# Kernel tuning notes

Hardware: AMD Instinct MI355X
Metric: run time of the kernel (lower is better)

Reference implementation:

```python
import jax, jax.numpy as jnp
import numpy as np

N, D = 4096, 512
TAU, ALPHA, EPS = 0.2, 0.5, 1e-15
L2_EPS = 1e-12  # F.normalize eps


def setup_inputs() -> dict:
    key = jax.random.key(0)
    ks = jax.random.split(key, 12)
    # xavier_normal_ with gain=1.414 for [D, D] linears
    std = 1.414 * (2.0 / (D + D)) ** 0.5
    xn = lambda k: jax.random.normal(k, (D, D), jnp.float32) * std
    return {
        "z1": jax.random.normal(ks[0], (N, D), jnp.float32),
        "z2": jax.random.normal(ks[1], (N, D), jnp.float32),
        # local projector: Linear -> PReLU -> Linear
        "lw1": xn(ks[2]), "lb1": jnp.zeros((D,), jnp.float32),
        "la": jnp.full((1,), 0.25, jnp.float32),  # PReLU weight (torch default 0.25)
        "lw2": xn(ks[3]), "lb2": jnp.zeros((D,), jnp.float32),
        # global projector
        "gw1": xn(ks[4]), "gb1": jnp.zeros((D,), jnp.float32),
        "ga": jnp.full((1,), 0.25, jnp.float32),
        "gw2": xn(ks[5]), "gb2": jnp.zeros((D,), jnp.float32),
        # discriminator bilinear weight
        "W": xn(ks[6]),
        # binary positive-pair mask [N, N]
        "mask": jax.random.randint(ks[7], (N, N), 0, 2, jnp.int32),
    }


def _prelu(x, a):
    return jnp.where(x >= 0, x, a * x)


def _proj(z, w1, b1, a, w2, b2):
    # nn.Sequential(Linear, PReLU, Linear); torch Linear: z @ W.T + b
    return _prelu(z @ w1.T + b1, a[0]) @ w2.T + b2


def _l2norm(z):
    n = jnp.linalg.norm(z, axis=-1, keepdims=True)
    return z / jnp.maximum(n, L2_EPS)


def _infonce(h1, h2, m, tau):
    a = _l2norm(h1)
    b = _l2norm(h2)
    sim_intra = jnp.exp(a @ a.T / tau)  # [N, N]
    sim_inter = jnp.exp(a @ b.T / tau)  # [N, N]
    num = (sim_inter * m).sum(1)
    den = sim_intra.sum(1) + sim_inter.sum(1) - (sim_intra * m).sum(1)
    return (-jnp.log(num / den)).mean()


def reference(z1, z2, lw1, lb1, la, lw2, lb2, gw1, gb1, ga, gw2, gb2, W, mask):
    m = mask.astype(jnp.float32)
    # local (node-level) InfoNCE through the local projector
    h1 = _proj(z1, lw1, lb1, la, lw2, lb2)
    h2 = _proj(z2, lw1, lb1, la, lw2, lb2)
    local = 0.5 * (_infonce(h1, h2, m, TAU) + _infonce(h2, h1, m.T, TAU))

    # global (DGI-style) loss
    def gloss(pos_z, neg_z):
        s = pos_z.mean(0)                               # readout [D]
        h = _proj(s, gw1, gb1, ga, gw2, gb2)            # global projector [D]
        summ = W @ h                                    # [D]
        d_pos = jax.nn.sigmoid(pos_z @ summ)            # [N]
        d_neg = jax.nn.sigmoid(neg_z @ summ)            # [N]
        pos_loss = -jnp.log(d_pos + EPS).mean()
        neg_loss = -jnp.log(1.0 - d_neg + EPS).mean()
        return 0.5 * (pos_loss + neg_loss)

    glob = 0.5 * (gloss(z1, z2) + gloss(z2, z1))
    return ALPHA * local + (1.0 - ALPHA) * glob
```

## Files before the change

kernel.cpp:

```cpp
#include <hip/hip_runtime.h>
#include <math.h>

#define NN 4096
#define DD 512
#define INV_TAU 5.0f
#define EPSV 1e-15f

typedef unsigned short u16;
typedef unsigned long long u64;
typedef __attribute__((ext_vector_type(8))) short short8;
typedef __attribute__((ext_vector_type(4))) float f32x4;

__device__ __forceinline__ void gld16(const void* g, void* l) {
  __builtin_amdgcn_global_load_lds(
      (const __attribute__((address_space(1))) unsigned int*)g,
      (__attribute__((address_space(3))) unsigned int*)l, 16, 0, 0);
}

__device__ __forceinline__ void bar_vm4() {
  asm volatile("s_waitcnt vmcnt(4) lgkmcnt(0)\n\ts_barrier" ::: "memory");
}
__device__ __forceinline__ void bar_vm2() {
  asm volatile("s_waitcnt vmcnt(2) lgkmcnt(0)\n\ts_barrier" ::: "memory");
}
__device__ __forceinline__ void bar_vm1() {
  asm volatile("s_waitcnt vmcnt(1) lgkmcnt(0)\n\ts_barrier" ::: "memory");
}
__device__ __forceinline__ void bar_vm0() {
  asm volatile("s_waitcnt vmcnt(0) lgkmcnt(0)\n\ts_barrier" ::: "memory");
}

__device__ __forceinline__ float bf2f(u16 u) {
  return __uint_as_float(((unsigned)u) << 16);
}
__device__ __forceinline__ u16 f2bf(float x) {
  unsigned u = __float_as_uint(x);
  u += 0x7fff + ((u >> 16) & 1);
  return (u16)(u >> 16);
}

__device__ __forceinline__ float wave_sum(float v) {
#pragma unroll
  for (int o = 32; o > 0; o >>= 1) v += __shfl_down(v, o, 64);
  return v;
}

__device__ __forceinline__ float ldz(const float* p) {
  return __hip_atomic_load(p, __ATOMIC_RELAXED, __HIP_MEMORY_SCOPE_AGENT);
}
__device__ __forceinline__ void stz(float* p, float v) {
  __hip_atomic_store(p, v, __ATOMIC_RELAXED, __HIP_MEMORY_SCOPE_AGENT);
}

__device__ __forceinline__ void fin_run(const float* zb, const float* plsP,
                                        const float* plsN, float* out,
                                        int tid) {
  const int lane = tid & 63, w = tid >> 6;
  float S1 = 0.f, S2 = 0.f;
#pragma unroll
  for (int k = 0; k < 8; ++k) {
    const int i = tid + k * 512;
    const float r11 = ldz(&zb[i]), r11m = ldz(&zb[NN + i]);
    const float r12 = ldz(&zb[2 * NN + i]), r12m = ldz(&zb[3 * NN + i]);
    const float c12 = ldz(&zb[4 * NN + i]), c12m = ldz(&zb[5 * NN + i]);
    const float c22 = ldz(&zb[6 * NN + i]), c22m = ldz(&zb[7 * NN + i]);
    S1 += -logf(r12m / (r11 + r12 - r11m));
    S2 += -logf(c12m / (c22 + c12 - c22m));
  }
  float G = (tid < 64) ? (ldz(&plsP[tid]) + ldz(&plsN[tid])) : 0.f;
  S1 = wave_sum(S1);
  S2 = wave_sum(S2);
  G = wave_sum(G);
  __shared__ float fr[3][8];
  if (lane == 0) { fr[0][w] = S1; fr[1][w] = S2; fr[2][w] = G; }
  __syncthreads();
  if (tid == 0) {
    float s1t = 0.f, s2t = 0.f, gt = 0.f;
    for (int q = 0; q < 8; ++q) {
      s1t += fr[0][q];
      s2t += fr[1][q];
      gt += fr[2][q];
    }
    const float local = 0.5f * (s1t + s2t) * (1.f / NN);
    const float glob = 0.25f * gt * (1.f / NN);
    out[0] = 0.5f * local + 0.5f * glob;
  }
}

__global__ __launch_bounds__(256) void tobf16cm(
    const float* __restrict__ a, const float* __restrict__ b,
    const float* __restrict__ c, const float* __restrict__ d2,
    u16* __restrict__ o, float* __restrict__ pc1, float* __restrict__ pc2,
    float* __restrict__ zbf, int* __restrict__ ctr) {
  const int bid = blockIdx.x, tid = threadIdx.x;
  if (bid >= 4608) {
    const int blk = bid - 4608;
    const int r0 = blk * 32;
    float a0 = 0.f, a1 = 0.f, c0 = 0.f, c1 = 0.f;
    for (int r = r0; r < r0 + 32; ++r) {
      const size_t ro = (size_t)r * DD;
      a0 += c[ro + tid];
      a1 += c[ro + 256 + tid];
      c0 += d2[ro + tid];
      c1 += d2[ro + 256 + tid];
    }
    pc1[blk * 512 + tid] = a0;
    pc1[blk * 512 + 256 + tid] = a1;
    pc2[blk * 512 + tid] = c0;
    pc2[blk * 512 + 256 + tid] = c1;
    return;
  }
  if (bid == 0 && tid == 0) ctr[0] = 0;
  if (bid < 128) zbf[bid * 256 + tid] = 0.f;
  const int i = bid * 256 + tid;
  int j = i;
  const float* s;
  if (j < 65536) {
    s = a + (size_t)j * 4;
  } else {
    j -= 65536;
    if (j < 65536) {
      s = b + (size_t)j * 4;
    } else {
      j -= 65536;
      if (j < 524288) {
        s = c + (size_t)j * 4;
      } else {
        j -= 524288;
        s = d2 + (size_t)j * 4;
      }
    }
  }
  float4 v = *(const float4*)s;
  u64 pk = (u64)f2bf(v.x) | ((u64)f2bf(v.y) << 16) | ((u64)f2bf(v.z) << 32) |
           ((u64)f2bf(v.w) << 48);
  *(u64*)&o[(size_t)i * 4] = pk;
}

template <int ACT>
__global__ __launch_bounds__(512) void gemm_mv(
    const u16* __restrict__ A, const u16* __restrict__ Bw,
    const float* __restrict__ bias, const float* __restrict__ alpha_p,
    u16* __restrict__ out, const float* __restrict__ Mw,
    const float* __restrict__ mx1, const float* __restrict__ mx2,
    const float* __restrict__ mbias, const float* __restrict__ mal,
    float* __restrict__ my1, float* __restrict__ my2) {
  __shared__ __align__(16) u16 sh[3 * 6144];
  __shared__ float svb[512];
  const int tid = threadIdx.x, w = tid >> 6, lane = tid & 63;
  if (blockIdx.x < 64) {
    const int mb = blockIdx.x;
    const int bz = mb >> 5, bx = mb & 31;
    const float* xin = bz ? mx2 : mx1;
    float* y = bz ? my2 : my1;
    if (ACT) {
      float a0 = 0.f, a1 = 0.f, a2 = 0.f, a3 = 0.f;
      for (int b = 0; b < 128; b += 4) {
        a0 += xin[b * 512 + tid];
        a1 += xin[(b + 1) * 512 + tid];
        a2 += xin[(b + 2) * 512 + tid];
        a3 += xin[(b + 3) * 512 + tid];
      }
      svb[tid] = ((a0 + a1) + (a2 + a3)) * (1.f / NN);
    } else {
      svb[tid] = xin[tid];
    }
    __syncthreads();
#pragma unroll
    for (int rr = 0; rr < 2; ++rr) {
      const int row = bx * 16 + w * 2 + rr;
      float acc = 0.f;
#pragma unroll
      for (int q = 0; q < 8; ++q)
        acc = fmaf(Mw[(size_t)row * DD + lane + 64 * q], svb[lane + 64 * q],
                   acc);
      acc = wave_sum(acc);
      if (lane == 0) {
        acc += mbias[row];
        if (ACT) {
          const float al = mal[0];
          acc = (acc >= 0.f) ? acc : al * acc;
        }
        y[row] = acc;
      }
    }
    return;
  }
  const int quad = lane >> 4, m16 = lane & 15;
  const int wi = w >> 1, wj = w & 1;
  const int bid2 = blockIdx.x - 64;
  const int xcd = bid2 & 7, idx = bid2 >> 3;
  const int i0 = (4 * xcd + (idx & 3)) * 128;
  const int j0 = ((idx >> 2) & 7) * 64;
  const int bz = idx >> 5;
  const u16* Ab = A + (size_t)bz * ((size_t)NN * DD);
  u16* ob = out + (size_t)bz * ((size_t)NN * DD);
  const int roff =
      (m16 >> 1) * 64 + (((((m16 & 1) << 2) | quad) ^ (m16 >> 1)) * 8);
  const int st = (lane & 7) ^ (lane >> 3);
  const int srow = 2 * (lane >> 3) + (st >> 2);
  const int scol = (st & 3) * 8;
  const u16* gs = (w < 4) ? Ab : Bw;
  const int grow0 = ((w < 4) ? i0 + 2 * w * 16 : j0 + (w - 4) * 16) + srow;
  const int doff0 = (w < 4) ? 2 * w * 512 : 4096 + (w - 4) * 512;
  auto stage = [&](int bo, int k) {
    const int kn = k * 32;
    gld16(&gs[(size_t)grow0 * DD + kn + scol], sh + bo + doff0);
    if (w < 4)
      gld16(&gs[(size_t)(grow0 + 16) * DD + kn + scol], sh + bo + doff0 + 512);
  };
  stage(0, 0);
  stage(6144, 1);
  if (w < 4) bar_vm2(); else bar_vm1();
  f32x4 acc[2][2] = {};
  int ro = 0;
  for (int kc = 0; kc < 16; ++kc) {
    if (kc <= 13) {
      int so = ro + 12288;
      if (so >= 18432) so -= 18432;
      stage(so, kc + 2);
    }
    const u16* As = sh + ro;
    const u16* Bs = sh + ro + 4096;
    short8 ar[2], br[2];
#pragma unroll
    for (int s = 0; s < 2; ++s) {
      ar[s] = *(const short8*)&As[(wi * 32 + s * 16) * 32 + roff];
      br[s] = *(const short8*)&Bs[(wj * 32 + s * 16) * 32 + roff];
    }
    __builtin_amdgcn_s_setprio(1);
#pragma unroll
    for (int si = 0; si < 2; ++si)
#pragma unroll
      for (int sj = 0; sj < 2; ++sj)
        acc[si][sj] = __builtin_amdgcn_mfma_f32_16x16x32_bf16(
            ar[si], br[sj], acc[si][sj], 0, 0, 0);
    __builtin_amdgcn_s_setprio(0);
    if (kc <= 13) {
      if (w < 4) bar_vm2(); else bar_vm1();
    } else if (kc == 14) {
      bar_vm0();
    }
    ro += 6144;
    if (ro == 18432) ro = 0;
  }
  const float al = ACT ? alpha_p[0] : 0.f;
#pragma unroll
  for (int si = 0; si < 2; ++si)
#pragma unroll
    for (int sj = 0; sj < 2; ++sj) {
      const int col = j0 + wj * 32 + sj * 16 + m16;
      const float bv = bias[col];
#pragma unroll
      for (int r = 0; r < 4; ++r) {
        const int row = i0 + wi * 32 + si * 16 + quad * 4 + r;
        float x = acc[si][sj][r] + bv;
        if (ACT) x = (x >= 0.f) ? x : al * x;
        ob[(size_t)row * DD + col] = f2bf(x);
      }
    }
}

__global__ __launch_bounds__(256) void rownorm_mv(
    const u16* __restrict__ h, u16* __restrict__ o,
    const float* __restrict__ W, const float* __restrict__ hx1,
    const float* __restrict__ hx2, float* __restrict__ sm1,
    float* __restrict__ sm2) {
  const int bid = blockIdx.x, tid = threadIdx.x;
  const int lane = tid & 63, w = tid >> 6;
  if (bid < 256) {
    const int bz = bid >> 7, bx = bid & 127;
    const float* x = bz ? hx2 : hx1;
    float* y = bz ? sm2 : sm1;
    const int row = bx * 4 + w;
    float acc = 0.f;
#pragma unroll
    for (int q = 0; q < 8; ++q)
      acc = fmaf(W[(size_t)row * DD + lane + 64 * q], x[lane + 64 * q], acc);
    acc = wave_sum(acc);
    if (lane == 0) y[row] = acc;
    return;
  }
  const int row = (bid - 256) * 4 + w;
  const size_t base = (size_t)row * DD + lane * 8;
  short8 v = *(const short8*)&h[base];
  float f[8];
  float s = 0.f;
#pragma unroll
  for (int j = 0; j < 8; ++j) {
    f[j] = bf2f((u16)v[j]);
    s += f[j] * f[j];
  }
  s = wave_sum(s);
  const float inv = 1.f / fmaxf(sqrtf(__shfl(s, 0, 64)), 1e-12f);
  short8 r;
#pragma unroll
  for (int j = 0; j < 8; ++j) r[j] = (short)f2bf(f[j] * inv);
  *(short8*)&o[base] = r;
}

__global__ __launch_bounds__(512) void sim_mfma(
    const u16* __restrict__ na, const u16* __restrict__ nb,
    const int* __restrict__ mask, float* __restrict__ zb,
    const float* __restrict__ z1g, const float* __restrict__ z2g,
    const float* __restrict__ sm1, const float* __restrict__ sm2,
    float* __restrict__ plsP, float* __restrict__ plsN,
    int* __restrict__ ctr, float* __restrict__ out) {
  extern __shared__ __align__(16) u16 shm[];
  __shared__ int lastf;
  const int tid = threadIdx.x;
  const int w = tid >> 6, lane = tid & 63;
  if (blockIdx.y < 2) {
    const int lx = blockIdx.y * 32 + blockIdx.x;
    const int bz = lx >> 5, bx5 = lx & 31;
    const float* z = bz ? z2g : z1g;
    const float* sp = bz ? sm2 : sm1;
    const float* sn = bz ? sm1 : sm2;
    float lp = 0.f, ln_ = 0.f;
    for (int k = 0; k < 16; ++k) {
      const int row = bx5 * 128 + w * 16 + k;
      float dp = 0.f, dn = 0.f;
#pragma unroll
      for (int t = 0; t < 8; ++t) {
        const float zv = z[(size_t)row * DD + lane + 64 * t];
        dp = fmaf(zv, sp[lane + 64 * t], dp);
        dn = fmaf(zv, sn[lane + 64 * t], dn);
      }
      dp = wave_sum(dp);
      dn = wave_sum(dn);
      if (lane == 0) {
        lp += -logf(1.f / (1.f + __expf(-dp)) + EPSV);
        ln_ += -logf(1.f - 1.f / (1.f + __expf(-dn)) + EPSV);
      }
    }
    float* red = (float*)shm;
    if (lane == 0) { red[w] = lp; red[8 + w] = ln_; }
    __syncthreads();
    if (tid == 0) {
      float sP = 0.f, sN = 0.f;
      for (int q = 0; q < 8; ++q) { sP += red[q]; sN += red[8 + q]; }
      stz(&plsP[lx], sP);
      stz(&plsN[lx], sN);
    }
    asm volatile("s_waitcnt vmcnt(0)" ::: "memory");
    __syncthreads();
    if (tid == 0) lastf = (atomicAdd(ctr, 1) == 1087) ? 1 : 0;
    __syncthreads();
    if (lastf) fin_run(zb, plsP, plsN, out, tid);
    return;
  }
  const int quad = lane >> 4, m16 = lane & 15;
  const int ig = w & 3, jh = w >> 2;
  const int i0 = (blockIdx.y - 2) * 128, j0 = blockIdx.x * 128;
  const int roff =
      (m16 >> 1) * 64 + (((((m16 & 1) << 2) | quad) ^ (m16 >> 1)) * 8);
  const int st = (lane & 7) ^ (lane >> 3);
  const int srow = 2 * (lane >> 3) + (st >> 2);
  const int scol = (st & 3) * 8;
  const int p = w >> 1, rh = (w & 1) * 64;
  const u16* gs = (p & 1) ? nb : na;
  const int gr = ((p < 2) ? i0 : j0) + rh + srow;
  u16* dst0 = shm + p * 4096 + rh * 32;
  auto stage = [&](int bo, int k) {
    const int kn = k * 32;
#pragma unroll
    for (int rr = 0; rr < 64; rr += 16)
      gld16(&gs[(size_t)(gr + rr) * DD + kn + scol], dst0 + bo + rr * 32);
  };
  stage(0, 0);
  stage(16384, 1);
  bar_vm4();
  f32x4 a11[2][4] = {}, a12[2][4] = {}, a22[2][4] = {};
  int ro = 0;
  for (int kc = 0; kc < 16; ++kc) {
    if (kc <= 13) {
      int so = ro + 32768;
      if (so >= 49152) so -= 49152;
      stage(so, kc + 2);
    }
    const u16* Ai = shm + ro;
    const u16* Bi = shm + ro + 4096;
    const u16* Aj = shm + ro + 8192;
    const u16* Bj = shm + ro + 12288;
    short8 ai0 = *(const short8*)&Ai[(ig * 32) * 32 + roff];
    short8 ai1 = *(const short8*)&Ai[(ig * 32 + 16) * 32 + roff];
    short8 bi0 = *(const short8*)&Bi[(ig * 32) * 32 + roff];
    short8 bi1 = *(const short8*)&Bi[(ig * 32 + 16) * 32 + roff];
#pragma unroll
    for (int c = 0; c < 4; ++c) {
      short8 aj = *(const short8*)&Aj[(jh * 64 + c * 16) * 32 + roff];
      short8 bj = *(const short8*)&Bj[(jh * 64 + c * 16) * 32 + roff];
      __builtin_amdgcn_s_setprio(1);
      a11[0][c] = __builtin_amdgcn_mfma_f32_16x16x32_bf16(ai0, aj, a11[0][c], 0, 0, 0);
      a11[1][c] = __builtin_amdgcn_mfma_f32_16x16x32_bf16(ai1, aj, a11[1][c], 0, 0, 0);
      a12[0][c] = __builtin_amdgcn_mfma_f32_16x16x32_bf16(ai0, bj, a12[0][c], 0, 0, 0);
      a12[1][c] = __builtin_amdgcn_mfma_f32_16x16x32_bf16(ai1, bj, a12[1][c], 0, 0, 0);
      a22[0][c] = __builtin_amdgcn_mfma_f32_16x16x32_bf16(bi0, bj, a22[0][c], 0, 0, 0);
      a22[1][c] = __builtin_amdgcn_mfma_f32_16x16x32_bf16(bi1, bj, a22[1][c], 0, 0, 0);
      __builtin_amdgcn_s_setprio(0);
    }
    if (kc <= 13) bar_vm4();
    else if (kc == 14) bar_vm0();
    ro += 16384;
    if (ro == 49152) ro = 0;
  }
  float* rred = (float*)(shm + 16384);
  float* cred = rred + 512;
  rred[tid] = 0.f;
  rred[tid + 512] = 0.f;
  __syncthreads();
  float rs11[2][4] = {}, rm11[2][4] = {}, rs12[2][4] = {}, rm12[2][4] = {};
  float cs12[4] = {}, cm12[4] = {}, cs22[4] = {}, cm22[4] = {};
#pragma unroll
  for (int t = 0; t < 2; ++t)
#pragma unroll
    for (int c = 0; c < 4; ++c) {
      const int gj = j0 + jh * 64 + c * 16 + m16;
#pragma unroll
      for (int r = 0; r < 4; ++r) {
        const int gi = i0 + ig * 32 + t * 16 + quad * 4 + r;
        const float mv = (float)mask[(size_t)gi * NN + gj];
        const float e11 = __expf(a11[t][c][r] * INV_TAU);
        const float e12 = __expf(a12[t][c][r] * INV_TAU);
        const float e22 = __expf(a22[t][c][r] * INV_TAU);
        rs11[t][r] += e11;
        rm11[t][r] += e11 * mv;
        rs12[t][r] += e12;
        rm12[t][r] += e12 * mv;
        cs12[c] += e12;
        cm12[c] += e12 * mv;
        cs22[c] += e22;
        cm22[c] += e22 * mv;
      }
    }
#pragma unroll
  for (int t = 0; t < 2; ++t)
#pragma unroll
    for (int r = 0; r < 4; ++r) {
      float v0 = rs11[t][r], v1 = rm11[t][r], v2 = rs12[t][r], v3 = rm12[t][r];
#pragma unroll
      for (int o = 1; o < 16; o <<= 1) {
        v0 += __shfl_xor(v0, o, 64);
        v1 += __shfl_xor(v1, o, 64);
        v2 += __shfl_xor(v2, o, 64);
        v3 += __shfl_xor(v3, o, 64);
      }
      if (m16 == 0) {
        const int il = ig * 32 + t * 16 + quad * 4 + r;
        atomicAdd(&rred[0 * 128 + il], v0);
        atomicAdd(&rred[1 * 128 + il], v1);
        atomicAdd(&rred[2 * 128 + il], v2);
        atomicAdd(&rred[3 * 128 + il], v3);
      }
    }
#pragma unroll
  for (int c = 0; c < 4; ++c) {
    float v0 = cs12[c], v1 = cm12[c], v2 = cs22[c], v3 = cm22[c];
    v0 += __shfl_xor(v0, 16, 64); v0 += __shfl_xor(v0, 32, 64);
    v1 += __shfl_xor(v1, 16, 64); v1 += __shfl_xor(v1, 32, 64);
    v2 += __shfl_xor(v2, 16, 64); v2 += __shfl_xor(v2, 32, 64);
    v3 += __shfl_xor(v3, 16, 64); v3 += __shfl_xor(v3, 32, 64);
    if (lane < 16) {
      const int jl = jh * 64 + c * 16 + lane;
      atomicAdd(&cred[0 * 128 + jl], v0);
      atomicAdd(&cred[1 * 128 + jl], v1);
      atomicAdd(&cred[2 * 128 + jl], v2);
      atomicAdd(&cred[3 * 128 + jl], v3);
    }
  }
  __syncthreads();
  if (tid < 128) {
#pragma unroll
    for (int q = 0; q < 4; ++q)
      atomicAdd(&zb[q * NN + i0 + tid], rred[q * 128 + tid]);
  } else if (tid < 256) {
    const int jl = tid - 128;
#pragma unroll
    for (int q = 0; q < 4; ++q)
      atomicAdd(&zb[(4 + q) * NN + j0 + jl], cred[q * 128 + jl]);
  }
  asm volatile("s_waitcnt vmcnt(0)" ::: "memory");
  __syncthreads();
  if (tid == 0) lastf = (atomicAdd(ctr, 1) == 1087) ? 1 : 0;
  __syncthreads();
  if (lastf) fin_run(zb, plsP, plsN, out, tid);
}

extern "C" void kernel_launch(void* const* d_in, const int* in_sizes, int n_in,
                              void* d_out, int out_size, void* d_ws,
                              size_t ws_size, hipStream_t stream) {
  const float* z1 = (const float*)d_in[0];
  const float* z2 = (const float*)d_in[1];
  const float* lw1 = (const float*)d_in[2];
  const float* lb1 = (const float*)d_in[3];
  const float* la = (const float*)d_in[4];
  const float* lw2 = (const float*)d_in[5];
  const float* lb2 = (const float*)d_in[6];
  const float* gw1 = (const float*)d_in[7];
  const float* gb1 = (const float*)d_in[8];
  const float* ga = (const float*)d_in[9];
  const float* gw2 = (const float*)d_in[10];
  const float* gb2 = (const float*)d_in[11];
  const float* W = (const float*)d_in[12];
  const int* mask = (const int*)d_in[13];
  float* out = (float*)d_out;

  static bool attr_set = false;
  if (!attr_set) {
    (void)hipFuncSetAttribute(reinterpret_cast<const void*>(sim_mfma),
                              hipFuncAttributeMaxDynamicSharedMemorySize,
                              98304);
    attr_set = true;
  }

  const size_t ND = (size_t)NN * DD;
  u16* W1b = (u16*)d_ws;
  u16* W2b = W1b + 512 * 512;
  u16* Ab = W1b + 2 * 512 * 512;
  u16* Bb = Ab + 2 * ND;
  float* zbf = (float*)(Bb + 2 * ND);
  float* pc1 = zbf + 8 * NN;
  float* pc2 = pc1 + 128 * 512;
  float* t1 = pc2 + 128 * 512;
  float* t2 = t1 + 512;
  float* hg1 = t2 + 512;
  float* hg2 = hg1 + 512;
  float* summ1 = hg2 + 512;
  float* summ2 = summ1 + 512;
  float* plsP = summ2 + 512;
  float* plsN = plsP + 64;
  int* ctr = (int*)(plsN + 64);

  tobf16cm<<<4736, dim3(256), 0, stream>>>(lw1, lw2, z1, z2, W1b, pc1, pc2,
                                           zbf, ctr);
  gemm_mv<1><<<576, dim3(512), 0, stream>>>(Ab, W1b, lb1, la, Bb, gw1, pc1,
                                            pc2, gb1, ga, t1, t2);
  gemm_mv<0><<<576, dim3(512), 0, stream>>>(Bb, W2b, lb2, la, Ab, gw2, t1, t2,
                                            gb2, nullptr, hg1, hg2);
  rownorm_mv<<<2304, dim3(256), 0, stream>>>(Ab, Bb, W, hg1, hg2, summ1,
                                             summ2);
  sim_mfma<<<dim3(32, 34), dim3(512), 98304, stream>>>(
      Bb, Bb + ND, mask, zbf, z1, z2, summ1, summ2, plsP, plsN, ctr, out);
}
```

Before: 260.0 us.

## Exploit symmetry of similarity matrices by computing only upper-triangular tile pairs

```diff
diff --git a/kernel.cpp b/kernel.cpp
--- a/kernel.cpp
+++ b/kernel.cpp
@@ -310,8 +310,9 @@
   __shared__ int lastf;
   const int tid = threadIdx.x;
   const int w = tid >> 6, lane = tid & 63;
-  if (blockIdx.y < 2) {
-    const int lx = blockIdx.y * 32 + blockIdx.x;
+  const int bid = blockIdx.x;
+  if (bid < 64) {
+    const int lx = bid;
     const int bz = lx >> 5, bx5 = lx & 31;
     const float* z = bz ? z2g : z1g;
     const float* sp = bz ? sm2 : sm1;
@@ -344,14 +345,19 @@
     }
     asm volatile("s_waitcnt vmcnt(0)" ::: "memory");
     __syncthreads();
-    if (tid == 0) lastf = (atomicAdd(ctr, 1) == 1087) ? 1 : 0;
+    if (tid == 0) lastf = (atomicAdd(ctr, 1) == 591) ? 1 : 0;
     __syncthreads();
     if (lastf) fin_run(zb, plsP, plsN, out, tid);
     return;
   }
+  const int tdec = bid - 64;
+  int bi = (int)(31.5f - sqrtf(31.5f * 31.5f - 2.f * (float)tdec + 0.25f));
+  while (bi > 0 && tdec < bi * 32 - (bi * (bi - 1)) / 2) --bi;
+  while (tdec >= (bi + 1) * 32 - ((bi + 1) * bi) / 2) ++bi;
+  const int bj = bi + (tdec - (bi * 32 - (bi * (bi - 1)) / 2));
+  const int i0 = bi * 128, j0 = bj * 128;
   const int quad = lane >> 4, m16 = lane & 15;
   const int ig = w & 3, jh = w >> 2;
-  const int i0 = (blockIdx.y - 2) * 128, j0 = blockIdx.x * 128;
   const int roff =
       (m16 >> 1) * 64 + (((((m16 & 1) << 2) | quad) ^ (m16 >> 1)) * 8);
   const int st = (lane & 7) ^ (lane >> 3);
@@ -370,7 +376,7 @@
   stage(0, 0);
   stage(16384, 1);
   bar_vm4();
-  f32x4 a11[2][4] = {}, a12[2][4] = {}, a22[2][4] = {};
+  f32x4 a11[2][4] = {}, a12[2][4] = {}, a21[2][4] = {}, a22[2][4] = {};
   int ro = 0;
   for (int kc = 0; kc < 16; ++kc) {
     if (kc <= 13) {
@@ -389,14 +395,16 @@
 #pragma unroll
     for (int c = 0; c < 4; ++c) {
       short8 aj = *(const short8*)&Aj[(jh * 64 + c * 16) * 32 + roff];
-      short8 bj = *(const short8*)&Bj[(jh * 64 + c * 16) * 32 + roff];
+      short8 bj2 = *(const short8*)&Bj[(jh * 64 + c * 16) * 32 + roff];
       __builtin_amdgcn_s_setprio(1);
       a11[0][c] = __builtin_amdgcn_mfma_f32_16x16x32_bf16(ai0, aj, a11[0][c], 0, 0, 0);
       a11[1][c] = __builtin_amdgcn_mfma_f32_16x16x32_bf16(ai1, aj, a11[1][c], 0, 0, 0);
-      a12[0][c] = __builtin_amdgcn_mfma_f32_16x16x32_bf16(ai0, bj, a12[0][c], 0, 0, 0);
-      a12[1][c] = __builtin_amdgcn_mfma_f32_16x16x32_bf16(ai1, bj, a12[1][c], 0, 0, 0);
-      a22[0][c] = __builtin_amdgcn_mfma_f32_16x16x32_bf16(bi0, bj, a22[0][c], 0, 0, 0);
-      a22[1][c] = __builtin_amdgcn_mfma_f32_16x16x32_bf16(bi1, bj, a22[1][c], 0, 0, 0);
+      a12[0][c] = __builtin_amdgcn_mfma_f32_16x16x32_bf16(ai0, bj2, a12[0][c], 0, 0, 0);
+      a12[1][c] = __builtin_amdgcn_mfma_f32_16x16x32_bf16(ai1, bj2, a12[1][c], 0, 0, 0);
+      a21[0][c] = __builtin_amdgcn_mfma_f32_16x16x32_bf16(bi0, aj, a21[0][c], 0, 0, 0);
+      a21[1][c] = __builtin_amdgcn_mfma_f32_16x16x32_bf16(bi1, aj, a21[1][c], 0, 0, 0);
+      a22[0][c] = __builtin_amdgcn_mfma_f32_16x16x32_bf16(bi0, bj2, a22[0][c], 0, 0, 0);
+      a22[1][c] = __builtin_amdgcn_mfma_f32_16x16x32_bf16(bi1, bj2, a22[1][c], 0, 0, 0);
       __builtin_amdgcn_s_setprio(0);
     }
     if (kc <= 13) bar_vm4();
@@ -404,84 +412,195 @@
     ro += 16384;
     if (ro == 49152) ro = 0;
   }
-  float* rred = (float*)(shm + 16384);
-  float* cred = rred + 512;
-  rred[tid] = 0.f;
-  rred[tid + 512] = 0.f;
-  __syncthreads();
-  float rs11[2][4] = {}, rm11[2][4] = {}, rs12[2][4] = {}, rm12[2][4] = {};
-  float cs12[4] = {}, cm12[4] = {}, cs22[4] = {}, cm22[4] = {};
-#pragma unroll
-  for (int t = 0; t < 2; ++t)
+  if (bi == bj) {
+    float* rred = (float*)(shm + 16384);
+    float* cred = rred + 512;
+    rred[tid] = 0.f;
+    rred[tid + 512] = 0.f;
+    __syncthreads();
+    float rs11[2][4] = {}, rm11[2][4] = {}, rs12[2][4] = {}, rm12[2][4] = {};
+    float cs12[4] = {}, cm12[4] = {}, cs22[4] = {}, cm22[4] = {};
+#pragma unroll
+    for (int t = 0; t < 2; ++t)
+#pragma unroll
+      for (int c = 0; c < 4; ++c) {
+        const int gj = j0 + jh * 64 + c * 16 + m16;
+#pragma unroll
+        for (int r = 0; r < 4; ++r) {
+          const int gi = i0 + ig * 32 + t * 16 + quad * 4 + r;
+          const float mv = (float)mask[(size_t)gi * NN + gj];
+          const float e11 = __expf(a11[t][c][r] * INV_TAU);
+          const float e12 = __expf(a12[t][c][r] * INV_TAU);
+          const float e22 = __expf(a22[t][c][r] * INV_TAU);
+          rs11[t][r] += e11;
+          rm11[t][r] += e11 * mv;
+          rs12[t][r] += e12;
+          rm12[t][r] += e12 * mv;
+          cs12[c] += e12;
+          cm12[c] += e12 * mv;
+          cs22[c] += e22;
+          cm22[c] += e22 * mv;
+        }
+      }
+#pragma unroll
+    for (int t = 0; t < 2; ++t)
+#pragma unroll
+      for (int r = 0; r < 4; ++r) {
+        float v0 = rs11[t][r], v1 = rm11[t][r], v2 = rs12[t][r],
+              v3 = rm12[t][r];
+#pragma unroll
+        for (int o = 1; o < 16; o <<= 1) {
+          v0 += __shfl_xor(v0, o, 64);
+          v1 += __shfl_xor(v1, o, 64);
+          v2 += __shfl_xor(v2, o, 64);
+          v3 += __shfl_xor(v3, o, 64);
+        }
+        if (m16 == 0) {
+          const int il = ig * 32 + t * 16 + quad * 4 + r;
+          atomicAdd(&rred[0 * 128 + il], v0);
+          atomicAdd(&rred[1 * 128 + il], v1);
+          atomicAdd(&rred[2 * 128 + il], v2);
+          atomicAdd(&rred[3 * 128 + il], v3);
+        }
+      }
 #pragma unroll
     for (int c = 0; c < 4; ++c) {
-      const int gj = j0 + jh * 64 + c * 16 + m16;
+      float v0 = cs12[c], v1 = cm12[c], v2 = cs22[c], v3 = cm22[c];
+      v0 += __shfl_xor(v0, 16, 64); v0 += __shfl_xor(v0, 32, 64);
+      v1 += __shfl_xor(v1, 16, 64); v1 += __shfl_xor(v1, 32, 64);
+      v2 += __shfl_xor(v2, 16, 64); v2 += __shfl_xor(v2, 32, 64);
+      v3 += __shfl_xor(v3, 16, 64); v3 += __shfl_xor(v3, 32, 64);
+      if (lane < 16) {
+        const int jl = jh * 64 + c * 16 + lane;
+        atomicAdd(&cred[0 * 128 + jl], v0);
+        atomicAdd(&cred[1 * 128 + jl], v1);
+        atomicAdd(&cred[2 * 128 + jl], v2);
+        atomicAdd(&cred[3 * 128 + jl], v3);
+      }
+    }
+    __syncthreads();
+    if (tid < 128) {
+#pragma unroll
+      for (int q = 0; q < 4; ++q)
+        atomicAdd(&zb[q * NN + i0 + tid], rred[q * 128 + tid]);
+    } else if (tid < 256) {
+      const int jl = tid - 128;
+#pragma unroll
+      for (int q = 0; q < 4; ++q)
+        atomicAdd(&zb[(4 + q) * NN + j0 + jl], cred[q * 128 + jl]);
+    }
+  } else {
+    float* rred = (float*)(shm + 16384);
+    float* cred = rred + 1024;
+    rred[tid] = 0.f;
+    rred[tid + 512] = 0.f;
+    rred[tid + 1024] = 0.f;
+    rred[tid + 1536] = 0.f;
+    __syncthreads();
+    float r0a[2][4] = {}, r1a[2][4] = {}, r2a[2][4] = {}, r3a[2][4] = {};
+    float r4a[2][4] = {}, r5a[2][4] = {}, r6a[2][4] = {}, r7a[2][4] = {};
+    float p0a[4] = {}, p1a[4] = {}, p2a[4] = {}, p3a[4] = {};
+    float p4a[4] = {}, p5a[4] = {}, p6a[4] = {}, p7a[4] = {};
+#pragma unroll
+    for (int t = 0; t < 2; ++t)
+#pragma unroll
+      for (int c = 0; c < 4; ++c) {
+        const int gj = j0 + jh * 64 + c * 16 + m16;
+#pragma unroll
+        for (int r = 0; r < 4; ++r) {
+          const int gi = i0 + ig * 32 + t * 16 + quad * 4 + r;
+          const float mv = (float)mask[(size_t)gi * NN + gj];
+          const float mvT = (float)mask[(size_t)gj * NN + gi];
+          const float e11 = __expf(a11[t][c][r] * INV_TAU);
+          const float e12 = __expf(a12[t][c][r] * INV_TAU);
+          const float e21 = __expf(a21[t][c][r] * INV_TAU);
+          const float e22 = __expf(a22[t][c][r] * INV_TAU);
+          r0a[t][r] += e11;
+          r1a[t][r] += e11 * mv;
+          r2a[t][r] += e12;
+          r3a[t][r] += e12 * mv;
+          r4a[t][r] += e21;
+          r5a[t][r] += e21 * mvT;
+          r6a[t][r] += e22;
+          r7a[t][r] += e22 * mvT;
+          p0a[c] += e11;
+          p1a[c] += e11 * mvT;
+          p2a[c] += e21;
+          p3a[c] += e21 * mvT;
+          p4a[c] += e12;
+          p5a[c] += e12 * mv;
+          p6a[c] += e22;
+          p7a[c] += e22 * mv;
+        }
+      }
+#pragma unroll
+    for (int t = 0; t < 2; ++t)
 #pragma unroll
       for (int r = 0; r < 4; ++r) {
-        const int gi = i0 + ig * 32 + t * 16 + quad * 4 + r;
-        const float mv = (float)mask[(size_t)gi * NN + gj];
-        const float e11 = __expf(a11[t][c][r] * INV_TAU);
-        const float e12 = __expf(a12[t][c][r] * INV_TAU);
-        const float e22 = __expf(a22[t][c][r] * INV_TAU);
-        rs11[t][r] += e11;
-        rm11[t][r] += e11 * mv;
-        rs12[t][r] += e12;
-        rm12[t][r] += e12 * mv;
-        cs12[c] += e12;
-        cm12[c] += e12 * mv;
-        cs22[c] += e22;
-        cm22[c] += e22 * mv;
-      }
-    }
-#pragma unroll
-  for (int t = 0; t < 2; ++t)
-#pragma unroll
-    for (int r = 0; r < 4; ++r) {
-      float v0 = rs11[t][r], v1 = rm11[t][r], v2 = rs12[t][r], v3 = rm12[t][r];
-#pragma unroll
-      for (int o = 1; o < 16; o <<= 1) {
-        v0 += __shfl_xor(v0, o, 64);
-        v1 += __shfl_xor(v1, o, 64);
-        v2 += __shfl_xor(v2, o, 64);
-        v3 += __shfl_xor(v3, o, 64);
-      }
-      if (m16 == 0) {
-        const int il = ig * 32 + t * 16 + quad * 4 + r;
-        atomicAdd(&rred[0 * 128 + il], v0);
-        atomicAdd(&rred[1 * 128 + il], v1);
-        atomicAdd(&rred[2 * 128 + il], v2);
-        atomicAdd(&rred[3 * 128 + il], v3);
-      }
-    }
-#pragma unroll
-  for (int c = 0; c < 4; ++c) {
-    float v0 = cs12[c], v1 = cm12[c], v2 = cs22[c], v3 = cm22[c];
-    v0 += __shfl_xor(v0, 16, 64); v0 += __shfl_xor(v0, 32, 64);
-    v1 += __shfl_xor(v1, 16, 64); v1 += __shfl_xor(v1, 32, 64);
-    v2 += __shfl_xor(v2, 16, 64); v2 += __shfl_xor(v2, 32, 64);
-    v3 += __shfl_xor(v3, 16, 64); v3 += __shfl_xor(v3, 32, 64);
-    if (lane < 16) {
-      const int jl = jh * 64 + c * 16 + lane;
-      atomicAdd(&cred[0 * 128 + jl], v0);
-      atomicAdd(&cred[1 * 128 + jl], v1);
-      atomicAdd(&cred[2 * 128 + jl], v2);
-      atomicAdd(&cred[3 * 128 + jl], v3);
-    }
-  }
-  __syncthreads();
-  if (tid < 128) {
-#pragma unroll
-    for (int q = 0; q < 4; ++q)
-      atomicAdd(&zb[q * NN + i0 + tid], rred[q * 128 + tid]);
-  } else if (tid < 256) {
-    const int jl = tid - 128;
-#pragma unroll
-    for (int q = 0; q < 4; ++q)
-      atomicAdd(&zb[(4 + q) * NN + j0 + jl], cred[q * 128 + jl]);
+        float v0 = r0a[t][r], v1 = r1a[t][r], v2 = r2a[t][r], v3 = r3a[t][r];
+        float v4 = r4a[t][r], v5 = r5a[t][r], v6 = r6a[t][r], v7 = r7a[t][r];
+#pragma unroll
+        for (int o = 1; o < 16; o <<= 1) {
+          v0 += __shfl_xor(v0, o, 64);
+          v1 += __shfl_xor(v1, o, 64);
+          v2 += __shfl_xor(v2, o, 64);
+          v3 += __shfl_xor(v3, o, 64);
+          v4 += __shfl_xor(v4, o, 64);
+          v5 += __shfl_xor(v5, o, 64);
+          v6 += __shfl_xor(v6, o, 64);
+          v7 += __shfl_xor(v7, o, 64);
+        }
+        if (m16 == 0) {
+          const int il = ig * 32 + t * 16 + quad * 4 + r;
+          atomicAdd(&rred[0 * 128 + il], v0);
+          atomicAdd(&rred[1 * 128 + il], v1);
+          atomicAdd(&rred[2 * 128 + il], v2);
+          atomicAdd(&rred[3 * 128 + il], v3);
+          atomicAdd(&rred[4 * 128 + il], v4);
+          atomicAdd(&rred[5 * 128 + il], v5);
+          atomicAdd(&rred[6 * 128 + il], v6);
+          atomicAdd(&rred[7 * 128 + il], v7);
+        }
+      }
+#pragma unroll
+    for (int c = 0; c < 4; ++c) {
+      float v0 = p0a[c], v1 = p1a[c], v2 = p2a[c], v3 = p3a[c];
+      float v4 = p4a[c], v5 = p5a[c], v6 = p6a[c], v7 = p7a[c];
+      v0 += __shfl_xor(v0, 16, 64); v0 += __shfl_xor(v0, 32, 64);
+      v1 += __shfl_xor(v1, 16, 64); v1 += __shfl_xor(v1, 32, 64);
+      v2 += __shfl_xor(v2, 16, 64); v2 += __shfl_xor(v2, 32, 64);
+      v3 += __shfl_xor(v3, 16, 64); v3 += __shfl_xor(v3, 32, 64);
+      v4 += __shfl_xor(v4, 16, 64); v4 += __shfl_xor(v4, 32, 64);
+      v5 += __shfl_xor(v5, 16, 64); v5 += __shfl_xor(v5, 32, 64);
+      v6 += __shfl_xor(v6, 16, 64); v6 += __shfl_xor(v6, 32, 64);
+      v7 += __shfl_xor(v7, 16, 64); v7 += __shfl_xor(v7, 32, 64);
+      if (lane < 16) {
+        const int jl = jh * 64 + c * 16 + lane;
+        atomicAdd(&cred[0 * 128 + jl], v0);
+        atomicAdd(&cred[1 * 128 + jl], v1);
+        atomicAdd(&cred[2 * 128 + jl], v2);
+        atomicAdd(&cred[3 * 128 + jl], v3);
+        atomicAdd(&cred[4 * 128 + jl], v4);
+        atomicAdd(&cred[5 * 128 + jl], v5);
+        atomicAdd(&cred[6 * 128 + jl], v6);
+        atomicAdd(&cred[7 * 128 + jl], v7);
+      }
+    }
+    __syncthreads();
+    if (tid < 128) {
+#pragma unroll
+      for (int q = 0; q < 8; ++q)
+        atomicAdd(&zb[q * NN + i0 + tid], rred[q * 128 + tid]);
+    } else if (tid < 256) {
+      const int jl = tid - 128;
+#pragma unroll
+      for (int q = 0; q < 8; ++q)
+        atomicAdd(&zb[q * NN + j0 + jl], cred[q * 128 + jl]);
+    }
   }
   asm volatile("s_waitcnt vmcnt(0)" ::: "memory");
   __syncthreads();
-  if (tid == 0) lastf = (atomicAdd(ctr, 1) == 1087) ? 1 : 0;
+  if (tid == 0) lastf = (atomicAdd(ctr, 1) == 591) ? 1 : 0;
   __syncthreads();
   if (lastf) fin_run(zb, plsP, plsN, out, tid);
 }
@@ -539,6 +658,6 @@
                                             gb2, nullptr, hg1, hg2);
   rownorm_mv<<<2304, dim3(256), 0, stream>>>(Ab, Bb, W, hg1, hg2, summ1,
                                              summ2);
-  sim_mfma<<<dim3(32, 34), dim3(512), 98304, stream>>>(
+  sim_mfma<<<dim3(592), dim3(512), 98304, stream>>>(
       Bb, Bb + ND, mask, zbf, z1, z2, summ1, summ2, plsP, plsN, ctr, out);
 }
```

After: 299.1 us. 15.0% more time.
